# Performance work log

Hardware: AMD Instinct MI355X
Metric: run time of the kernel (lower is better)

## Reference

```python
import jax, jax.numpy as jnp
import numpy as np
from jax import lax

V, E, H, B, S, L, T = 30000, 300, 256, 32, 256, 4, 9
H2 = 2 * H            # bidirectional encoder output / decoder hidden
DIN = 2 * H2 + L      # decoder LSTM input size


def setup_inputs() -> dict:
    key = jax.random.key(0)
    ks = jax.random.split(key, 14)
    rn = lambda k, shp, s=0.05: (jax.random.normal(k, shp, dtype=jnp.float32) * s)
    return {
        "seqs": jax.random.randint(ks[0], (B, S), 0, V, dtype=jnp.int32),
        "emb": rn(ks[1], (V, E)),
        "enc_Wih_f": rn(ks[2], (4 * H, E)),
        "enc_Whh_f": rn(ks[3], (4 * H, H)),
        "enc_b_f": rn(ks[4], (4 * H,)),
        "enc_Wih_b": rn(ks[5], (4 * H, E)),
        "enc_Whh_b": rn(ks[6], (4 * H, H)),
        "enc_b_b": rn(ks[7], (4 * H,)),
        "W_att": rn(ks[8], (H2, H2)),
        "dec_Wih": rn(ks[9], (4 * H2, DIN)),
        "dec_Whh": rn(ks[10], (4 * H2, H2)),
        "dec_b": rn(ks[11], (4 * H2,)),
        "W_tag": rn(ks[12], (T, H2)),
        "b_tag": rn(ks[13], (T,)),
    }


def _lstm_scan(x_seq, Wih, Whh, b, hidden):
    """x_seq: [S,B,Din] -> outputs [S,B,hidden]. PyTorch gate order i,f,g,o."""
    nb = x_seq.shape[1]
    h0 = jnp.zeros((nb, hidden), x_seq.dtype)
    c0 = jnp.zeros((nb, hidden), x_seq.dtype)

    def step(carry, x):
        h, c = carry
        g = x @ Wih.T + h @ Whh.T + b
        i, f, gg, o = jnp.split(g, 4, axis=-1)
        c = jax.nn.sigmoid(f) * c + jax.nn.sigmoid(i) * jnp.tanh(gg)
        h = jax.nn.sigmoid(o) * jnp.tanh(c)
        return (h, c), h

    _, hs = lax.scan(step, (h0, c0), x_seq)
    return hs


def reference(seqs, emb, enc_Wih_f, enc_Whh_f, enc_b_f, enc_Wih_b, enc_Whh_b,
              enc_b_b, W_att, dec_Wih, dec_Whh, dec_b, W_tag, b_tag):
    # embed and transpose to [S, B, E]
    x = jnp.transpose(emb[seqs], (1, 0, 2))
    # bidirectional encoder LSTM -> h: [S, B, 2H]
    h_f = _lstm_scan(x, enc_Wih_f, enc_Whh_f, enc_b_f, H)
    h_b = jnp.flip(_lstm_scan(jnp.flip(x, 0), enc_Wih_b, enc_Whh_b, enc_b_b, H), 0)
    h = jnp.concatenate([h_f, h_b], axis=-1)

    # precompute W_att @ h (same math as per-step linear in original)
    Wh = jnp.einsum('sbh,oh->sbo', h, W_att)   # [S,B,H2]

    s0 = jnp.zeros((B, H2), x.dtype)
    c0 = jnp.zeros((B, H2), x.dtype)

    def decode_level(carry, onehot):           # onehot: [L]
        def step(carry2, h_t):                 # h_t: [B,H2]
            s, c = carry2
            score = jnp.einsum('sbo,bo->bs', Wh, s)       # [B,S]
            att = jax.nn.softmax(score, axis=1)
            ctx = jnp.einsum('sbh,bs->bh', h, att)        # [B,H2]
            xin = jnp.concatenate(
                [ctx, h_t, jnp.broadcast_to(onehot, (B, L))], axis=-1)
            g = xin @ dec_Wih.T + s @ dec_Whh.T + dec_b
            i, f, gg, o = jnp.split(g, 4, axis=-1)
            c = jax.nn.sigmoid(f) * c + jax.nn.sigmoid(i) * jnp.tanh(gg)
            s = jax.nn.sigmoid(o) * jnp.tanh(c)
            return (s, c), s

        carry, outs = lax.scan(step, carry, h)  # outs: [S,B,H2]
        return carry, outs

    # state (s,c) persists across nested levels, matching the original loop
    _, all_outs = lax.scan(decode_level, (s0, c0), jnp.eye(L, dtype=x.dtype))
    # [L,S,B,H2] -> tag scores [L,S,B,T]
    return jnp.einsum('lsbh,th->lsbt', all_outs, W_tag) + b_tag
```

## Files before the change

### kernel.cpp

```cpp
#include <hip/hip_runtime.h>
#include <cstdint>
#include <cstddef>

using u16 = unsigned short;
using u32 = unsigned int;

typedef __attribute__((ext_vector_type(8))) __bf16 bf16x8;
typedef __attribute__((ext_vector_type(4))) float f32x4;

__device__ __forceinline__ float bf2f(u16 u){
  union { u32 i; float f; } v; v.i = ((u32)u) << 16; return v.f;
}
__device__ __forceinline__ u16 f2bf(float f){
  union { float f; u32 i; } v; v.f = f;
  return (u16)((v.i + 0x7FFFu + ((v.i >> 16) & 1u)) >> 16);
}
__device__ __forceinline__ float sigm(float x){ return 1.0f / (1.0f + __expf(-x)); }
__device__ __forceinline__ f32x4 mfma16(bf16x8 a, bf16x8 b, f32x4 c){
  return __builtin_amdgcn_mfma_f32_16x16x32_bf16(a, b, c, 0, 0, 0);
}
__device__ __forceinline__ float ldin(const void* p, size_t i, bool f){
  return f ? ((const float*)p)[i] : bf2f(((const u16*)p)[i]);
}

__device__ __forceinline__ uint4 ldx4_cg(const u16* p){
  uint4 r;
  asm volatile("global_load_dwordx4 %0, %1, off sc0 sc1" : "=v"(r) : "v"(p) : "memory");
  return r;
}
__device__ __forceinline__ void st16_cg(u16* p, u32 v){
  asm volatile("global_store_short %0, %1, off sc0 sc1" :: "v"(p), "v"(v) : "memory");
}
__device__ __forceinline__ void wait_vm0(){ asm volatile("s_waitcnt vmcnt(0)" ::: "memory"); }

__device__ __forceinline__ void bar_arrive(u32* bar){
  __hip_atomic_fetch_add(bar, 1u, __ATOMIC_RELAXED, __HIP_MEMORY_SCOPE_AGENT);
}
__device__ __forceinline__ void bar_spin(u32* bar, u32 tgt){
  while (__hip_atomic_load(bar, __ATOMIC_RELAXED, __HIP_MEMORY_SCOPE_AGENT) < tgt)
    __builtin_amdgcn_s_sleep(1);
}

__global__ __launch_bounds__(256) void k_detect(const u32* __restrict__ embw, u32* __restrict__ dflag){
  int tid = threadIdx.x;
  u32 cnt = 0;
  for (int t = 0; t < 32; ++t){
    u32 w = embw[t*256 + tid];
    u32 e = (w >> 7) & 0xFFu;
    cnt += (e >= 0xC0u) ? 1u : 0u;
  }
  atomicAdd(dflag, cnt);
}


__global__ __launch_bounds__(256) void k_pack(
  const void* eWihF, const void* eWihB, const void* ebF, const void* ebB,
  const void* dWih, const void* dWhh, const void* db, const void* Wtag,
  const void* eWhhF, const void* eWhhB, const void* Watt, const void* btag,
  const u32* __restrict__ dflag,
  u16* __restrict__ WihCat, float* __restrict__ bcat, u16* __restrict__ WihH,
  u16* __restrict__ Wf, float* __restrict__ lbv, u16* __restrict__ WtagP,
  u16* __restrict__ WhhFb, u16* __restrict__ WhhBb, u16* __restrict__ Wattb,
  float* __restrict__ btagf)
{
  bool isf = (*dflag > 64u);
  long i = (long)blockIdx.x * 256 + threadIdx.x;
  if (i < 655360){
    long n = i / 320, e = i - n*320;
    WihCat[i] = (e < 300)
      ? f2bf(ldin(n < 1024 ? eWihF : eWihB, (size_t)(n & 1023)*300 + e, isf)) : (u16)0;
    return;
  }
  i -= 655360;
  if (i < 2048){ bcat[i] = ldin(i < 1024 ? ebF : ebB, (size_t)(i & 1023), isf); return; }
  i -= 2048;
  if (i < 1048576){
    long n = i >> 9, k = i & 511;
    WihH[i] = f2bf(ldin(dWih, (size_t)n*1028 + 512 + k, isf));
    return;
  }
  i -= 1048576;
  if (i < 2097152){
    long e  = i & 7;
    long ln = (i >> 3) & 63;
    long kt = (i >> 9) & 31;
    long rt = (i >> 14) & 3;
    long wgi = i >> 16;
    long n = rt*512 + wgi*16 + (ln & 15);
    long k = kt*32 + (ln >> 4)*8 + e;
    Wf[i] = f2bf((k < 512) ? ldin(dWih, (size_t)n*1028 + k, isf)
                           : ldin(dWhh, (size_t)n*512 + (k - 512), isf));
    return;
  }
  i -= 2097152;
  if (i < 8192){
    long l = i >> 11, n = i & 2047;
    lbv[i] = ldin(db, n, isf) + ldin(dWih, (size_t)n*1028 + 1024 + l, isf);
    return;
  }
  i -= 8192;
  if (i < 8192){
    long n = i >> 9, k = i & 511;
    WtagP[i] = (n < 9) ? f2bf(ldin(Wtag, (size_t)n*512 + k, isf)) : (u16)0;
    return;
  }
  i -= 8192;
  if (i < 262144){ WhhFb[i] = f2bf(ldin(eWhhF, i, isf)); return; }
  i -= 262144;
  if (i < 262144){ WhhBb[i] = f2bf(ldin(eWhhB, i, isf)); return; }
  i -= 262144;
  if (i < 262144){ Wattb[i] = f2bf(ldin(Watt, i, isf)); return; }
  i -= 262144;
  if (i < 16){ btagf[i] = (i < 9) ? ldin(btag, i, isf) : 0.f; return; }
}

__global__ __launch_bounds__(256) void k_gather(
  const int* __restrict__ seqs, const void* __restrict__ emb,
  const u32* __restrict__ dflag, u16* __restrict__ X)
{
  bool isf = (*dflag > 64u);
  int idx = blockIdx.x * 256 + threadIdx.x;
  if (idx >= 8192*320) return;
  int row = idx / 320, e = idx - row*320;
  int s = row >> 5, b = row & 31;
  int tok = seqs[b*256 + s];
  X[idx] = (e < 300) ? f2bf(ldin(emb, (size_t)tok*300 + e, isf)) : (u16)0;
}


__global__ __launch_bounds__(256) void k_gemm(
  const u16* __restrict__ A, const u16* __restrict__ B, const float* __restrict__ bias,
  u16* __restrict__ C, int M, int N, int K)
{
  int mb = blockIdx.x * 32;
  int wave = threadIdx.x >> 6, lane = threadIdx.x & 63;
  int nb = blockIdx.y * 256 + wave * 64;
  int rlo = lane & 15, klane = (lane >> 4) * 8;
  f32x4 acc[2][4];
  #pragma unroll
  for (int i = 0; i < 2; ++i)
    #pragma unroll
    for (int j = 0; j < 4; ++j) acc[i][j] = (f32x4){0,0,0,0};
  for (int kk = 0; kk < K; kk += 32){
    bf16x8 a0 = *(const bf16x8*)(A + (size_t)(mb + rlo)*K + kk + klane);
    bf16x8 a1 = *(const bf16x8*)(A + (size_t)(mb + 16 + rlo)*K + kk + klane);
    #pragma unroll
    for (int nt = 0; nt < 4; ++nt){
      bf16x8 bv = *(const bf16x8*)(B + (size_t)(nb + nt*16 + rlo)*K + kk + klane);
      acc[0][nt] = mfma16(a0, bv, acc[0][nt]);
      acc[1][nt] = mfma16(a1, bv, acc[1][nt]);
    }
  }
  int rbase = (lane >> 4) * 4;
  #pragma unroll
  for (int mt = 0; mt < 2; ++mt)
    #pragma unroll
    for (int nt = 0; nt < 4; ++nt){
      int col = nb + nt*16 + rlo;
      float badd = bias ? bias[col] : 0.0f;
      #pragma unroll
      for (int r = 0; r < 4; ++r){
        int row = mb + mt*16 + rbase + r;
        C[(size_t)row*N + col] = f2bf(acc[mt][nt][r] + badd);
      }
    }
}


__global__ __launch_bounds__(256) void k_transp(const u16* __restrict__ hglob, u16* __restrict__ hT)
{
  __shared__ u16 tile_t[64][264];
  int b = blockIdx.x >> 3, d0 = (blockIdx.x & 7) * 64;
  int t = threadIdx.x;
  for (int rr = 0; rr < 16; ++rr){
    int c = rr*256 + t;
    int j = c >> 4, dq = (c & 15) * 4;
    ushort4 ld = *(const ushort4*)(hglob + ((size_t)(j*32 + b)*512 + d0 + dq));
    tile_t[dq + 0][j] = ld.x;
    tile_t[dq + 1][j] = ld.y;
    tile_t[dq + 2][j] = ld.z;
    tile_t[dq + 3][j] = ld.w;
  }
  __syncthreads();
  for (int rr = 0; rr < 8; ++rr){
    int c = rr*256 + t;
    int d = c >> 5, jq = (c & 31) * 8;
    *(uint4*)(hT + ((size_t)(b*512 + d0 + d)*256 + jq)) = *(const uint4*)&tile_t[d][jq];
  }
}


__global__ __launch_bounds__(256, 1) void k_encoder(
  const u16* __restrict__ XW, const u16* __restrict__ WhhF, const u16* __restrict__ WhhB,
  u16* __restrict__ hglob, u16* __restrict__ hstate, u32* ctrlE)
{
  int wg = blockIdx.x;
  int d = wg >> 4, w = wg & 15;
  const u16* Whh = d ? WhhB : WhhF;
  u32* bar = ctrlE + d * 256;
  int tid = threadIdx.x, wave = tid >> 6, lane = tid & 63;
  int cc = lane & 15, q = lane >> 4, klane = q * 8, rbase = q * 4;
  __shared__ __align__(16) u16 hblk[8192];
  __shared__ float g_lds[4][32][16];
  __shared__ float c_sh[512];
  c_sh[tid] = 0.f; c_sh[tid + 256] = 0.f;
  __syncthreads();

  for (int t = 0; t < 256; ++t){
    int srow = d ? (255 - t) : t;
    const u16* hr = hstate + (size_t)(d*2 + (t & 1)) * 8192;
    u16*       hw = hstate + (size_t)(d*2 + ((t & 1) ^ 1)) * 8192;

    {
      int c0 = tid, c1 = tid + 256, c2 = tid + 512, c3 = tid + 768;
      uint4 v0 = ldx4_cg(hr + (c0 >> 5)*256 + (c0 & 31)*8);
      uint4 v1 = ldx4_cg(hr + (c1 >> 5)*256 + (c1 & 31)*8);
      uint4 v2 = ldx4_cg(hr + (c2 >> 5)*256 + (c2 & 31)*8);
      uint4 v3 = ldx4_cg(hr + (c3 >> 5)*256 + (c3 & 31)*8);
      wait_vm0();
      *(uint4*)(hblk + (c0 >> 5)*256 + (((c0 & 31) ^ ((c0 >> 5) & 7)))*8) = v0;
      *(uint4*)(hblk + (c1 >> 5)*256 + (((c1 & 31) ^ ((c1 >> 5) & 7)))*8) = v1;
      *(uint4*)(hblk + (c2 >> 5)*256 + (((c2 & 31) ^ ((c2 >> 5) & 7)))*8) = v2;
      *(uint4*)(hblk + (c3 >> 5)*256 + (((c3 & 31) ^ ((c3 >> 5) & 7)))*8) = v3;
    }
    __syncthreads();

    {
      int ncol = wave*256 + w*16 + cc;
      const u16* Brow = Whh + (size_t)ncol*256;
      f32x4 acc0 = {0,0,0,0}, acc1 = {0,0,0,0};
      #pragma unroll
      for (int kt = 0; kt < 8; ++kt){
        bf16x8 bv = *(const bf16x8*)(Brow + kt*32 + klane);
        bf16x8 a0 = *(const bf16x8*)(hblk + cc*256 + ((kt*4 + q) ^ (cc & 7))*8);
        bf16x8 a1 = *(const bf16x8*)(hblk + (cc + 16)*256 + ((kt*4 + q) ^ (cc & 7))*8);
        acc0 = mfma16(a0, bv, acc0);
        acc1 = mfma16(a1, bv, acc1);
      }
      #pragma unroll
      for (int r = 0; r < 4; ++r){
        g_lds[wave][rbase + r][cc]      = acc0[r];
        g_lds[wave][16 + rbase + r][cc] = acc1[r];
      }
    }
    __syncthreads();

    for (int e = tid; e < 512; e += 256){
      int b_ = e >> 4, jc = e & 15;
      int j = w*16 + jc;
      float pre[4];
      #pragma unroll
      for (int g2 = 0; g2 < 4; ++g2)
        pre[g2] = g_lds[g2][b_][jc] + bf2f(XW[(size_t)(srow*32 + b_)*2048 + d*1024 + g2*256 + j]);
      float iv = sigm(pre[0]), fv = sigm(pre[1]);
      float gv = tanhf(pre[2]), ov = sigm(pre[3]);
      float cv = fv * c_sh[e] + iv * gv;
      c_sh[e] = cv;
      u16 hb = f2bf(ov * tanhf(cv));
      st16_cg(hw + b_*256 + j, (u32)hb);
      __builtin_nontemporal_store(hb, hglob + (size_t)(srow*32 + b_)*512 + d*256 + j);
    }
    wait_vm0();
    __syncthreads();
    if (tid == 0){
      bar_arrive(bar);
      bar_spin(bar, (u32)(t + 1) * 16u);
    }
    __syncthreads();
  }
}


__global__ __launch_bounds__(512, 1) void k_decoder(
  const u16* __restrict__ Whb, const u16* __restrict__ hT,
  const u16* __restrict__ Wf, const u16* __restrict__ Xh, const float* __restrict__ lbv,
  u16* __restrict__ Ain,
  u16* __restrict__ aouts,
  u32* bar1, u32* bar2)
{
  extern __shared__ __align__(16) u16 ablk[];
  __shared__ float score_lds[256];
  __shared__ __align__(16) u16 att_bf[256];
  __shared__ float gbuf[4][16][33];
  __shared__ float c_lds[512];
  const int wg = blockIdx.x, tid = threadIdx.x;
  const int wave = tid >> 6, lane = tid & 63;
  const int q = lane >> 4, cc = lane & 15;
  c_lds[tid] = 0.0f;

  bf16x8 wh[2][16];
  #pragma unroll
  for (int rt = 0; rt < 2; ++rt)
    #pragma unroll
    for (int kt = 0; kt < 16; ++kt){
      int row = wave*32 + rt*16 + cc;
      wh[rt][kt] = *(const bf16x8*)(Whb + ((size_t)(row*32 + wg))*512 + kt*32 + q*8);
    }
  const int grt = wave >> 1, gct = wave & 1;
  const int bcol = gct*16 + cc;
  const u16* WfW = Wf + (size_t)wg*65536;
  const int pb_ = tid >> 4, pdd = tid & 15;
  const int pgj = wg*16 + pdd;
  float lb[4];
  __syncthreads();

  for (int iter = 0; iter < 1024; ++iter){
    const int l = iter >> 8, t = iter & 255;
    u16* AinC = Ain + (iter & 1)*32768;
    u16* AinN = Ain + ((iter & 1) ^ 1)*32768;

    {
      int c0 = tid, c1 = tid + 512, c2 = tid + 1024, c3 = tid + 1536;
      uint4 v0 = ldx4_cg(AinC + (c0 >> 6)*1024 + 512 + (c0 & 63)*8);
      uint4 v1 = ldx4_cg(AinC + (c1 >> 6)*1024 + 512 + (c1 & 63)*8);
      uint4 v2 = ldx4_cg(AinC + (c2 >> 6)*1024 + 512 + (c2 & 63)*8);
      uint4 v3 = ldx4_cg(AinC + (c3 >> 6)*1024 + 512 + (c3 & 63)*8);
      wait_vm0();
      *(uint4*)(ablk + (c0 >> 6)*1024 + (64 + ((c0 & 63) ^ ((c0 >> 6) & 7)))*8) = v0;
      *(uint4*)(ablk + (c1 >> 6)*1024 + (64 + ((c1 & 63) ^ ((c1 >> 6) & 7)))*8) = v1;
      *(uint4*)(ablk + (c2 >> 6)*1024 + (64 + ((c2 & 63) ^ ((c2 >> 6) & 7)))*8) = v2;
      *(uint4*)(ablk + (c3 >> 6)*1024 + (64 + ((c3 & 63) ^ ((c3 >> 6) & 7)))*8) = v3;
    }
    __syncthreads();

    if ((iter & 255) == 0){
      #pragma unroll
      for (int g = 0; g < 4; ++g) lb[g] = lbv[l*2048 + g*512 + pgj];
    }
    float xh[4];
    #pragma unroll
    for (int g = 0; g < 4; ++g) xh[g] = bf2f(Xh[(size_t)(t*32 + pb_)*2048 + g*512 + pgj]);

    f32x4 sa0 = {0,0,0,0}, sa1 = {0,0,0,0};
    #pragma unroll
    for (int kt = 0; kt < 16; ++kt){
      bf16x8 sv = *(const bf16x8*)(ablk + wg*1024 + ((64 + kt*4 + q) ^ (wg & 7))*8);
      sa0 = mfma16(wh[0][kt], sv, sa0);
      sa1 = mfma16(wh[1][kt], sv, sa1);
    }
    if (cc == 0){
      #pragma unroll
      for (int r = 0; r < 4; ++r){
        score_lds[wave*32      + q*4 + r] = sa0[r];
        score_lds[wave*32 + 16 + q*4 + r] = sa1[r];
      }
    }
    __syncthreads();

    if (wave == 0){
      float x0 = score_lds[lane*4+0], x1 = score_lds[lane*4+1];
      float x2 = score_lds[lane*4+2], x3 = score_lds[lane*4+3];
      float m = fmaxf(fmaxf(x0,x1), fmaxf(x2,x3));
      #pragma unroll
      for (int off = 32; off >= 1; off >>= 1) m = fmaxf(m, __shfl_xor(m, off));
      float e0 = __expf(x0-m), e1 = __expf(x1-m), e2 = __expf(x2-m), e3 = __expf(x3-m);
      float s = e0+e1+e2+e3;
      #pragma unroll
      for (int off = 32; off >= 1; off >>= 1) s += __shfl_xor(s, off);
      float inv = 1.0f / s;
      att_bf[lane*4+0] = f2bf(e0*inv);
      att_bf[lane*4+1] = f2bf(e1*inv);
      att_bf[lane*4+2] = f2bf(e2*inv);
      att_bf[lane*4+3] = f2bf(e3*inv);
    }
    __syncthreads();

    f32x4 ca0 = {0,0,0,0}, ca1 = {0,0,0,0}, ca2 = {0,0,0,0}, ca3 = {0,0,0,0};
    #pragma unroll
    for (int jt = 0; jt < 8; ++jt){
      uint4 au = {0,0,0,0};
      if (cc == 0) au = *(const uint4*)(att_bf + jt*32 + q*8);
      bf16x8 af = *(bf16x8*)&au;
      const u16* hb = hT + ((size_t)(wg*512 + wave*64 + cc))*256 + jt*32 + q*8;
      ca0 = mfma16(af, *(const bf16x8*)(hb +  0*256), ca0);
      ca1 = mfma16(af, *(const bf16x8*)(hb + 16*256), ca1);
      ca2 = mfma16(af, *(const bf16x8*)(hb + 32*256), ca2);
      ca3 = mfma16(af, *(const bf16x8*)(hb + 48*256), ca3);
    }
    if (q == 0){
      u16* dst = AinC + wg*1024 + wave*64 + cc;
      st16_cg(dst +  0, (u32)f2bf(ca0[0]));
      st16_cg(dst + 16, (u32)f2bf(ca1[0]));
      st16_cg(dst + 32, (u32)f2bf(ca2[0]));
      st16_cg(dst + 48, (u32)f2bf(ca3[0]));
    }
    wait_vm0();
    __syncthreads();
    if (tid == 0) bar_arrive(bar2);

    f32x4 ga = {0,0,0,0};
    #pragma unroll
    for (int kt = 16; kt < 32; ++kt){
      bf16x8 wa = *(const bf16x8*)(WfW + ((grt*32 + kt)*64 + lane)*8);
      bf16x8 av = *(const bf16x8*)(ablk + bcol*1024 + ((kt*4 + q) ^ (bcol & 7))*8);
      ga = mfma16(wa, av, ga);
    }
    if (tid == 0) bar_spin(bar2, 32u*(u32)(iter+1));
    __syncthreads();

    {
      int c0 = tid, c1 = tid + 512, c2 = tid + 1024, c3 = tid + 1536;
      uint4 v0 = ldx4_cg(AinC + (c0 >> 6)*1024 + (c0 & 63)*8);
      uint4 v1 = ldx4_cg(AinC + (c1 >> 6)*1024 + (c1 & 63)*8);
      uint4 v2 = ldx4_cg(AinC + (c2 >> 6)*1024 + (c2 & 63)*8);
      uint4 v3 = ldx4_cg(AinC + (c3 >> 6)*1024 + (c3 & 63)*8);
      wait_vm0();
      *(uint4*)(ablk + (c0 >> 6)*1024 + (((c0 & 63) ^ ((c0 >> 6) & 7)))*8) = v0;
      *(uint4*)(ablk + (c1 >> 6)*1024 + (((c1 & 63) ^ ((c1 >> 6) & 7)))*8) = v1;
      *(uint4*)(ablk + (c2 >> 6)*1024 + (((c2 & 63) ^ ((c2 >> 6) & 7)))*8) = v2;
      *(uint4*)(ablk + (c3 >> 6)*1024 + (((c3 & 63) ^ ((c3 >> 6) & 7)))*8) = v3;
    }
    __syncthreads();

    #pragma unroll
    for (int kt = 0; kt < 16; ++kt){
      bf16x8 wa = *(const bf16x8*)(WfW + ((grt*32 + kt)*64 + lane)*8);
      bf16x8 av = *(const bf16x8*)(ablk + bcol*1024 + ((kt*4 + q) ^ (bcol & 7))*8);
      ga = mfma16(wa, av, ga);
    }
    #pragma unroll
    for (int r = 0; r < 4; ++r) gbuf[grt][q*4 + r][bcol] = ga[r];
    __syncthreads();

    {
      float pre[4];
      #pragma unroll
      for (int g = 0; g < 4; ++g)
        pre[g] = gbuf[g][pdd][pb_] + xh[g] + lb[g];
      float iv = sigm(pre[0]), fv = sigm(pre[1]);
      float gv = tanhf(pre[2]), ov = sigm(pre[3]);
      float cv = fv * c_lds[tid] + iv * gv;
      c_lds[tid] = cv;
      u16 hb = f2bf(ov * tanhf(cv));
      st16_cg(AinN + pb_*1024 + 512 + pgj, (u32)hb);
      __builtin_nontemporal_store(hb, aouts + (size_t)((l*256 + t)*32 + pb_)*512 + pgj);
    }
    wait_vm0();
    __syncthreads();
    if (tid == 0){
      bar_arrive(bar1);
      bar_spin(bar1, 32u*(u32)(iter+1));
    }
    __syncthreads();
  }
}


__global__ __launch_bounds__(256) void k_tag(
  const u16* __restrict__ aouts, const u16* __restrict__ WtagP, const float* __restrict__ btagf,
  const u32* __restrict__ dflag, void* __restrict__ out)
{
  bool isf = (*dflag > 64u);
  int wave = threadIdx.x >> 6, lane = threadIdx.x & 63;
  int mb = (blockIdx.x * 4 + wave) * 16;
  int cc = lane & 15, klane = (lane >> 4) * 8;
  f32x4 acc = {0,0,0,0};
  const u16* Arow = aouts + (size_t)(mb + cc)*512;
  const u16* Brow = WtagP + cc*512;
  #pragma unroll
  for (int kk = 0; kk < 512; kk += 32){
    bf16x8 av = *(const bf16x8*)(Arow + kk + klane);
    bf16x8 bv = *(const bf16x8*)(Brow + kk + klane);
    acc = mfma16(av, bv, acc);
  }
  int rbase = (lane >> 4) * 4;
  if (cc < 9){
    float bt = btagf[cc];
    #pragma unroll
    for (int r = 0; r < 4; ++r){
      int row = mb + rbase + r;
      float v = acc[r] + bt;
      if (isf) ((float*)out)[(size_t)row*9 + cc] = v;
      else     ((u16*)out)[(size_t)row*9 + cc] = f2bf(v);
    }
  }
}


extern "C" void kernel_launch(void* const* d_in, const int* in_sizes, int n_in,
                              void* d_out, int out_size, void* d_ws, size_t ws_size,
                              hipStream_t stream)
{
  (void)in_sizes; (void)n_in; (void)out_size;
  if (ws_size < 98625536ull) return;

  const int* seqs = (const int*)d_in[0];

  char* ws = (char*)d_ws;
  u32*    dflag  = (u32*)(ws + 0);
  u32*    barEF  = (u32*)(ws + 1024);
  u32*    barD1  = (u32*)(ws + 3072);
  u32*    barD2  = (u32*)(ws + 4096);
  u16*    Ain    = (u16*)(ws + 8192);
  u16*    hstate = (u16*)(ws + 139264);
  u16*    WihCat = (u16*)(ws + 263168);
  float*  bcat   = (float*)(ws + 1573888);
  u16*    WihH   = (u16*)(ws + 1582080);
  u16*    Wf     = (u16*)(ws + 3679232);
  float*  lbv    = (float*)(ws + 7873536);
  u16*    WtagP  = (u16*)(ws + 7906304);
  u16*    WhhFb  = (u16*)(ws + 7922688);
  u16*    WhhBb  = (u16*)(ws + 8446976);
  u16*    Wattb  = (u16*)(ws + 8971264);
  float*  btagf  = (float*)(ws + 9495552);
  u16*    X      = (u16*)(ws + 9496576);
  u16*    XWXh   = (u16*)(ws + 14739456);
  u16*    aouts  = (u16*)(ws + 48293888);
  u16*    hglob  = (u16*)(ws + 48293888);
  u16*    hT     = (u16*)(ws + 81848320);
  u16*    Whb    = (u16*)(ws + 90236928);

  hipMemsetAsync(d_ws, 0, 204800, stream);

  k_detect<<<1, 256, 0, stream>>>((const u32*)d_in[1], dflag);
  k_pack<<<17993, 256, 0, stream>>>(
      d_in[2], d_in[5], d_in[4], d_in[7], d_in[9], d_in[10], d_in[11], d_in[12],
      d_in[3], d_in[6], d_in[8], d_in[13], dflag,
      WihCat, bcat, WihH, Wf, lbv, WtagP, WhhFb, WhhBb, Wattb, btagf);
  k_gather<<<10240, 256, 0, stream>>>(seqs, d_in[1], dflag, X);
  k_gemm<<<dim3(256, 8), 256, 0, stream>>>(X, WihCat, bcat, XWXh, 8192, 2048, 320);
  k_encoder<<<32, 256, 0, stream>>>(XWXh, WhhFb, WhhBb, hglob, hstate, barEF);
  k_gemm<<<dim3(256, 2), 256, 0, stream>>>(hglob, Wattb, nullptr, Whb, 8192, 512, 512);
  k_gemm<<<dim3(256, 8), 256, 0, stream>>>(hglob, WihH, nullptr, XWXh, 8192, 2048, 512);
  k_transp<<<256, 256, 0, stream>>>(hglob, hT);

  k_decoder<<<32, 512, 65536, stream>>>(Whb, hT, Wf, XWXh, lbv, Ain, aouts, barD1, barD2);
  k_tag<<<512, 256, 0, stream>>>(aouts, WtagP, btagf, dflag, d_out);
}
```

Measured before the change: 23.05 ms.

## Split decoder into four independent batch groups with per-group barriers

Repartitions the decoder gate GEMM so each of 4 groups of 8 workgroups handles 8 batch rows and all 2048 gate outputs for a 64-wide hidden slice. Grid barriers now span 8 blocks instead of 32, and each block stages only 8 batch rows into LDS instead of 32. Wf packing is changed to match the new layout. The aim is to cut barrier latency and global-to-LDS traffic on each sequential step. In exchange each block streams 4x more weight data per step and half the MFMA columns are zero-padded.

```diff
diff --git a/kernel.cpp b/kernel.cpp
--- a/kernel.cpp
+++ b/kernel.cpp
@@ -6,6 +6,7 @@
 using u32 = unsigned int;
 
 typedef __attribute__((ext_vector_type(8))) __bf16 bf16x8;
+typedef __attribute__((ext_vector_type(8))) short short8;
 typedef __attribute__((ext_vector_type(4))) float f32x4;
 
 __device__ __forceinline__ float bf2f(u16 u){
@@ -84,9 +85,11 @@
     long e  = i & 7;
     long ln = (i >> 3) & 63;
     long kt = (i >> 9) & 31;
-    long rt = (i >> 14) & 3;
-    long wgi = i >> 16;
-    long n = rt*512 + wgi*16 + (ln & 15);
+    long rt = (i >> 14) & 15;
+    long w  = (i >> 18) & 7;
+    long rl = rt*16 + (ln & 15);
+    long g2 = rl >> 6, d = rl & 63;
+    long n = g2*512 + w*64 + d;
     long k = kt*32 + (ln >> 4)*8 + e;
     Wf[i] = f2bf((k < 512) ? ldin(dWih, (size_t)n*1028 + k, isf)
                            : ldin(dWhh, (size_t)n*512 + (k - 512), isf));
@@ -276,16 +279,19 @@
   const u16* __restrict__ Wf, const u16* __restrict__ Xh, const float* __restrict__ lbv,
   u16* __restrict__ Ain,
   u16* __restrict__ aouts,
-  u32* bar1, u32* bar2)
-{
-  extern __shared__ __align__(16) u16 ablk[];
+  u32* barD)
+{
+  __shared__ __align__(16) u16 ablk[8*1024];
   __shared__ float score_lds[256];
   __shared__ __align__(16) u16 att_bf[256];
-  __shared__ float gbuf[4][16][33];
+  __shared__ float gbuf[256][9];
   __shared__ float c_lds[512];
   const int wg = blockIdx.x, tid = threadIdx.x;
+  const int grp = wg >> 3, w = wg & 7;
   const int wave = tid >> 6, lane = tid & 63;
   const int q = lane >> 4, cc = lane & 15;
+  u32* bar2 = barD + grp*128;
+  u32* bar1 = barD + grp*128 + 64;
   c_lds[tid] = 0.0f;
 
   bf16x8 wh[2][16];
@@ -296,45 +302,39 @@
       int row = wave*32 + rt*16 + cc;
       wh[rt][kt] = *(const bf16x8*)(Whb + ((size_t)(row*32 + wg))*512 + kt*32 + q*8);
     }
-  const int grt = wave >> 1, gct = wave & 1;
-  const int bcol = gct*16 + cc;
-  const u16* WfW = Wf + (size_t)wg*65536;
-  const int pb_ = tid >> 4, pdd = tid & 15;
-  const int pgj = wg*16 + pdd;
+  const u16* WfW = Wf + (size_t)w*262144;
+  const int rt0 = wave*2, rt1 = wave*2 + 1;
+  const int pb_ = tid >> 6, pdd = tid & 63;
   float lb[4];
   __syncthreads();
 
   for (int iter = 0; iter < 1024; ++iter){
     const int l = iter >> 8, t = iter & 255;
+    const u32 e = (u32)(iter + 1);
     u16* AinC = Ain + (iter & 1)*32768;
     u16* AinN = Ain + ((iter & 1) ^ 1)*32768;
 
     {
-      int c0 = tid, c1 = tid + 512, c2 = tid + 1024, c3 = tid + 1536;
-      uint4 v0 = ldx4_cg(AinC + (c0 >> 6)*1024 + 512 + (c0 & 63)*8);
-      uint4 v1 = ldx4_cg(AinC + (c1 >> 6)*1024 + 512 + (c1 & 63)*8);
-      uint4 v2 = ldx4_cg(AinC + (c2 >> 6)*1024 + 512 + (c2 & 63)*8);
-      uint4 v3 = ldx4_cg(AinC + (c3 >> 6)*1024 + 512 + (c3 & 63)*8);
+      int row = tid >> 6, ch = tid & 63;
+      uint4 v = ldx4_cg(AinC + (size_t)(grp*8 + row)*1024 + 512 + ch*8);
       wait_vm0();
-      *(uint4*)(ablk + (c0 >> 6)*1024 + (64 + ((c0 & 63) ^ ((c0 >> 6) & 7)))*8) = v0;
-      *(uint4*)(ablk + (c1 >> 6)*1024 + (64 + ((c1 & 63) ^ ((c1 >> 6) & 7)))*8) = v1;
-      *(uint4*)(ablk + (c2 >> 6)*1024 + (64 + ((c2 & 63) ^ ((c2 >> 6) & 7)))*8) = v2;
-      *(uint4*)(ablk + (c3 >> 6)*1024 + (64 + ((c3 & 63) ^ ((c3 >> 6) & 7)))*8) = v3;
+      *(uint4*)(ablk + row*1024 + 512 + ((ch ^ (row & 7)))*8) = v;
     }
     __syncthreads();
 
     if ((iter & 255) == 0){
       #pragma unroll
-      for (int g = 0; g < 4; ++g) lb[g] = lbv[l*2048 + g*512 + pgj];
+      for (int g = 0; g < 4; ++g) lb[g] = lbv[l*2048 + g*512 + w*64 + pdd];
     }
     float xh[4];
     #pragma unroll
-    for (int g = 0; g < 4; ++g) xh[g] = bf2f(Xh[(size_t)(t*32 + pb_)*2048 + g*512 + pgj]);
+    for (int g = 0; g < 4; ++g)
+      xh[g] = bf2f(Xh[(size_t)(t*32 + grp*8 + pb_)*2048 + g*512 + w*64 + pdd]);
 
     f32x4 sa0 = {0,0,0,0}, sa1 = {0,0,0,0};
     #pragma unroll
     for (int kt = 0; kt < 16; ++kt){
-      bf16x8 sv = *(const bf16x8*)(ablk + wg*1024 + ((64 + kt*4 + q) ^ (wg & 7))*8);
+      bf16x8 sv = *(const bf16x8*)(ablk + w*1024 + 512 + (((kt*4 + q) ^ (w & 7)))*8);
       sa0 = mfma16(wh[0][kt], sv, sa0);
       sa1 = mfma16(wh[1][kt], sv, sa1);
     }
@@ -378,7 +378,7 @@
       ca3 = mfma16(af, *(const bf16x8*)(hb + 48*256), ca3);
     }
     if (q == 0){
-      u16* dst = AinC + wg*1024 + wave*64 + cc;
+      u16* dst = AinC + (size_t)wg*1024 + wave*64 + cc;
       st16_cg(dst +  0, (u32)f2bf(ca0[0]));
       st16_cg(dst + 16, (u32)f2bf(ca1[0]));
       st16_cg(dst + 32, (u32)f2bf(ca2[0]));
@@ -388,58 +388,62 @@
     __syncthreads();
     if (tid == 0) bar_arrive(bar2);
 
-    f32x4 ga = {0,0,0,0};
+    f32x4 ga0 = {0,0,0,0}, ga1 = {0,0,0,0};
     #pragma unroll
     for (int kt = 16; kt < 32; ++kt){
-      bf16x8 wa = *(const bf16x8*)(WfW + ((grt*32 + kt)*64 + lane)*8);
-      bf16x8 av = *(const bf16x8*)(ablk + bcol*1024 + ((kt*4 + q) ^ (bcol & 7))*8);
-      ga = mfma16(wa, av, ga);
-    }
-    if (tid == 0) bar_spin(bar2, 32u*(u32)(iter+1));
+      bf16x8 bv = (bf16x8)(short8){0,0,0,0,0,0,0,0};
+      if (cc < 8)
+        bv = *(const bf16x8*)(ablk + cc*1024 + 512 + ((((kt-16)*4 + q) ^ (cc & 7)))*8);
+      ga0 = mfma16(*(const bf16x8*)(WfW + (rt0*32 + kt)*512 + lane*8), bv, ga0);
+      ga1 = mfma16(*(const bf16x8*)(WfW + (rt1*32 + kt)*512 + lane*8), bv, ga1);
+    }
+    if (tid == 0) bar_spin(bar2, 8u*e);
     __syncthreads();
 
     {
-      int c0 = tid, c1 = tid + 512, c2 = tid + 1024, c3 = tid + 1536;
-      uint4 v0 = ldx4_cg(AinC + (c0 >> 6)*1024 + (c0 & 63)*8);
-      uint4 v1 = ldx4_cg(AinC + (c1 >> 6)*1024 + (c1 & 63)*8);
-      uint4 v2 = ldx4_cg(AinC + (c2 >> 6)*1024 + (c2 & 63)*8);
-      uint4 v3 = ldx4_cg(AinC + (c3 >> 6)*1024 + (c3 & 63)*8);
+      int row = tid >> 6, ch = tid & 63;
+      uint4 v = ldx4_cg(AinC + (size_t)(grp*8 + row)*1024 + ch*8);
       wait_vm0();
-      *(uint4*)(ablk + (c0 >> 6)*1024 + (((c0 & 63) ^ ((c0 >> 6) & 7)))*8) = v0;
-      *(uint4*)(ablk + (c1 >> 6)*1024 + (((c1 & 63) ^ ((c1 >> 6) & 7)))*8) = v1;
-      *(uint4*)(ablk + (c2 >> 6)*1024 + (((c2 & 63) ^ ((c2 >> 6) & 7)))*8) = v2;
-      *(uint4*)(ablk + (c3 >> 6)*1024 + (((c3 & 63) ^ ((c3 >> 6) & 7)))*8) = v3;
+      *(uint4*)(ablk + row*1024 + ((ch ^ (row & 7)))*8) = v;
     }
     __syncthreads();
 
     #pragma unroll
     for (int kt = 0; kt < 16; ++kt){
-      bf16x8 wa = *(const bf16x8*)(WfW + ((grt*32 + kt)*64 + lane)*8);
-      bf16x8 av = *(const bf16x8*)(ablk + bcol*1024 + ((kt*4 + q) ^ (bcol & 7))*8);
-      ga = mfma16(wa, av, ga);
-    }
-    #pragma unroll
-    for (int r = 0; r < 4; ++r) gbuf[grt][q*4 + r][bcol] = ga[r];
+      bf16x8 bv = (bf16x8)(short8){0,0,0,0,0,0,0,0};
+      if (cc < 8)
+        bv = *(const bf16x8*)(ablk + cc*1024 + (((kt*4 + q) ^ (cc & 7)))*8);
+      ga0 = mfma16(*(const bf16x8*)(WfW + (rt0*32 + kt)*512 + lane*8), bv, ga0);
+      ga1 = mfma16(*(const bf16x8*)(WfW + (rt1*32 + kt)*512 + lane*8), bv, ga1);
+    }
+    if (cc < 8){
+      #pragma unroll
+      for (int r = 0; r < 4; ++r){
+        gbuf[rt0*16 + q*4 + r][cc] = ga0[r];
+        gbuf[rt1*16 + q*4 + r][cc] = ga1[r];
+      }
+    }
     __syncthreads();
 
     {
       float pre[4];
       #pragma unroll
       for (int g = 0; g < 4; ++g)
-        pre[g] = gbuf[g][pdd][pb_] + xh[g] + lb[g];
+        pre[g] = gbuf[g*64 + pdd][pb_] + xh[g] + lb[g];
       float iv = sigm(pre[0]), fv = sigm(pre[1]);
       float gv = tanhf(pre[2]), ov = sigm(pre[3]);
       float cv = fv * c_lds[tid] + iv * gv;
       c_lds[tid] = cv;
       u16 hb = f2bf(ov * tanhf(cv));
-      st16_cg(AinN + pb_*1024 + 512 + pgj, (u32)hb);
-      __builtin_nontemporal_store(hb, aouts + (size_t)((l*256 + t)*32 + pb_)*512 + pgj);
+      st16_cg(AinN + (size_t)(grp*8 + pb_)*1024 + 512 + w*64 + pdd, (u32)hb);
+      __builtin_nontemporal_store(hb,
+          aouts + (size_t)((l*256 + t)*32 + grp*8 + pb_)*512 + w*64 + pdd);
     }
     wait_vm0();
     __syncthreads();
     if (tid == 0){
       bar_arrive(bar1);
-      bar_spin(bar1, 32u*(u32)(iter+1));
+      bar_spin(bar1, 8u*e);
     }
     __syncthreads();
   }
@@ -488,11 +492,10 @@
 
   char* ws = (char*)d_ws;
   u32*    dflag  = (u32*)(ws + 0);
-  u32*    barEF  = (u32*)(ws + 1024);
-  u32*    barD1  = (u32*)(ws + 3072);
-  u32*    barD2  = (u32*)(ws + 4096);
-  u16*    Ain    = (u16*)(ws + 8192);
-  u16*    hstate = (u16*)(ws + 139264);
+  u32*    barD   = (u32*)(ws + 4096);
+  u32*    ctrlE  = (u32*)(ws + 12288);
+  u16*    Ain    = (u16*)(ws + 16384);
+  u16*    hstate = (u16*)(ws + 147456);
   u16*    WihCat = (u16*)(ws + 263168);
   float*  bcat   = (float*)(ws + 1573888);
   u16*    WihH   = (u16*)(ws + 1582080);
@@ -510,7 +513,7 @@
   u16*    hT     = (u16*)(ws + 81848320);
   u16*    Whb    = (u16*)(ws + 90236928);
 
-  hipMemsetAsync(d_ws, 0, 204800, stream);
+  hipMemsetAsync(d_ws, 0, 212992, stream);
 
   k_detect<<<1, 256, 0, stream>>>((const u32*)d_in[1], dflag);
   k_pack<<<17993, 256, 0, stream>>>(
@@ -519,11 +522,11 @@
       WihCat, bcat, WihH, Wf, lbv, WtagP, WhhFb, WhhBb, Wattb, btagf);
   k_gather<<<10240, 256, 0, stream>>>(seqs, d_in[1], dflag, X);
   k_gemm<<<dim3(256, 8), 256, 0, stream>>>(X, WihCat, bcat, XWXh, 8192, 2048, 320);
-  k_encoder<<<32, 256, 0, stream>>>(XWXh, WhhFb, WhhBb, hglob, hstate, barEF);
+  k_encoder<<<32, 256, 0, stream>>>(XWXh, WhhFb, WhhBb, hglob, hstate, ctrlE);
   k_gemm<<<dim3(256, 2), 256, 0, stream>>>(hglob, Wattb, nullptr, Whb, 8192, 512, 512);
   k_gemm<<<dim3(256, 8), 256, 0, stream>>>(hglob, WihH, nullptr, XWXh, 8192, 2048, 512);
   k_transp<<<256, 256, 0, stream>>>(hglob, hT);
 
-  k_decoder<<<32, 512, 65536, stream>>>(Whb, hT, Wf, XWXh, lbv, Ain, aouts, barD1, barD2);
+  k_decoder<<<32, 512, 0, stream>>>(Whb, hT, Wf, XWXh, lbv, Ain, aouts, barD);
   k_tag<<<512, 256, 0, stream>>>(aouts, WtagP, btagf, dflag, d_out);
 }
```

Result: slower. 28.97 ms (+25.6%).
